# Kernel tuning notes

Hardware: AMD Instinct MI355X
Metric: run time of the kernel (lower is better)

The kernel has to match this reference:

```python
import jax, jax.numpy as jnp
import numpy as np

BATCH = 262144
LATENT_DIM = 128
N_CLUSTERS = 10


def setup_inputs() -> dict:
    key = jax.random.key(0)
    kz, kc = jax.random.split(key)
    z = jax.random.normal(kz, (BATCH, LATENT_DIM), dtype=jnp.float32)
    cluster_centers = jax.random.normal(kc, (N_CLUSTERS, LATENT_DIM), dtype=jnp.float32)
    return {"z": z, "cluster_centers": cluster_centers}


def reference(z, cluster_centers):
    # Student's-t soft assignment (alpha = 1):
    # q_ij = (1 + ||z_i - mu_j||^2)^-1, power ((alpha+1)/2) == 1
    # squared distances: [B, K]
    sq_dist = jnp.sum(jnp.square(z[:, None, :] - cluster_centers[None, :, :]), axis=2)
    q = 1.0 / (1.0 + sq_dist)
    q = q ** ((1.0 + 1.0) / 2.0)
    q = q / jnp.sum(q, axis=1, keepdims=True)  # row-normalize

    # target distribution p
    weight = q ** 2 / jnp.sum(q, axis=0)            # [B, K] / [K]
    p = weight / jnp.sum(weight, axis=1, keepdims=True)
    return (q, p)
```

## Files before the change

kernel.cpp:

```cpp
#include <hip/hip_runtime.h>
#include <stdint.h>

#define NB 262144
#define D 128
#define K 10

#define QBLOCKS 2048
#define QTHREADS 256
#define QITERS (NB * 4 / (QBLOCKS * QTHREADS))

__global__ __launch_bounds__(QTHREADS) void qkern(
    const float* __restrict__ z, const float* __restrict__ centers,
    float* __restrict__ qout, float* __restrict__ f) {
  __shared__ float c_lds[K * D];
  __shared__ float red[4][K];

  const int t = threadIdx.x;
  const int w = t >> 6;
  const int lane = t & 63;

  for (int i = t; i < K * D; i += QTHREADS) c_lds[i] = centers[i];
  __syncthreads();

  float colp[K];
#pragma unroll
  for (int j = 0; j < K; ++j) colp[j] = 0.f;

  for (int it = 0; it < QITERS; ++it) {
    const int g = (blockIdx.x + it * QBLOCKS) * QTHREADS + t;
    const int r = g >> 2;
    const int sub = g & 3;

    float acc[K];
#pragma unroll
    for (int j = 0; j < K; ++j) acc[j] = 0.f;

    const float* zr = z + (size_t)r * D + sub * 4;
#pragma unroll
    for (int k = 0; k < 8; ++k) {
      float4 zv = *reinterpret_cast<const float4*>(&zr[k * 16]);
#pragma unroll
      for (int j = 0; j < K; ++j) {
        float4 cv = *reinterpret_cast<const float4*>(&c_lds[j * D + k * 16 + sub * 4]);
        float dx = zv.x - cv.x; acc[j] = fmaf(dx, dx, acc[j]);
        float dy = zv.y - cv.y; acc[j] = fmaf(dy, dy, acc[j]);
        float dz = zv.z - cv.z; acc[j] = fmaf(dz, dz, acc[j]);
        float dw = zv.w - cv.w; acc[j] = fmaf(dw, dw, acc[j]);
      }
    }
#pragma unroll
    for (int j = 0; j < K; ++j) {
      acc[j] += __shfl_xor(acc[j], 1);
      acc[j] += __shfl_xor(acc[j], 2);
    }

    if (sub == 0) {
      float qu[K];
      float srow = 0.f;
#pragma unroll
      for (int j = 0; j < K; ++j) {
        qu[j] = 1.0f / (1.0f + acc[j]);
        srow += qu[j];
      }
      float inv = 1.0f / srow;
#pragma unroll
      for (int j = 0; j < K; ++j) {
        qu[j] *= inv;
        colp[j] += qu[j];
      }
      float* qo = qout + (size_t)r * K;
      *reinterpret_cast<float4*>(&qo[0]) = make_float4(qu[0], qu[1], qu[2], qu[3]);
      *reinterpret_cast<float4*>(&qo[4]) = make_float4(qu[4], qu[5], qu[6], qu[7]);
      *reinterpret_cast<float2*>(&qo[8]) = make_float2(qu[8], qu[9]);
    }
  }

#pragma unroll
  for (int j = 0; j < K; ++j) {
    colp[j] += __shfl_xor(colp[j], 4);
    colp[j] += __shfl_xor(colp[j], 8);
    colp[j] += __shfl_xor(colp[j], 16);
    colp[j] += __shfl_xor(colp[j], 32);
  }
  if (lane == 0) {
#pragma unroll
    for (int j = 0; j < K; ++j) red[w][j] = colp[j];
  }
  __syncthreads();
  if (t < K) {
    float s = red[0][t] + red[1][t] + red[2][t] + red[3][t];
    atomicAdd(&f[t], s);
  }
}

__global__ __launch_bounds__(256) void pkern(
    const float* __restrict__ q, const float* __restrict__ f,
    float* __restrict__ p) {
  int row = blockIdx.x * 256 + threadIdx.x;
  const float* qr = q + (size_t)row * K;
  float wv[K];
  float s = 0.f;
#pragma unroll
  for (int j = 0; j < K; j += 2) {
    float2 qq = *reinterpret_cast<const float2*>(&qr[j]);
    wv[j] = qq.x * qq.x / f[j];
    wv[j + 1] = qq.y * qq.y / f[j + 1];
    s += wv[j] + wv[j + 1];
  }
  float inv = 1.0f / s;
  float* pr = p + (size_t)row * K;
#pragma unroll
  for (int j = 0; j < K; j += 2) {
    *reinterpret_cast<float2*>(&pr[j]) = make_float2(wv[j] * inv, wv[j + 1] * inv);
  }
}

extern "C" void kernel_launch(void* const* d_in, const int* in_sizes, int n_in,
                              void* d_out, int out_size, void* d_ws, size_t ws_size,
                              hipStream_t stream) {
  const float* z = (const float*)d_in[0];
  const float* centers = (const float*)d_in[1];
  float* out = (float*)d_out;
  float* f = (float*)d_ws;

  hipMemsetAsync(d_ws, 0, K * sizeof(float), stream);
  qkern<<<QBLOCKS, QTHREADS, 0, stream>>>(z, centers, out, f);
  pkern<<<NB / 256, 256, 0, stream>>>(out, f, out + (size_t)NB * K);
}
```

Measured before the change: 252.4 us.

## Compute cluster distances with bf16 MFMA via norm expansion

```diff
diff --git a/kernel.cpp b/kernel.cpp
--- a/kernel.cpp
+++ b/kernel.cpp
@@ -5,92 +5,112 @@
 #define D 128
 #define K 10
 
-#define QBLOCKS 2048
+#define QBLOCKS 1024
 #define QTHREADS 256
-#define QITERS (NB * 4 / (QBLOCKS * QTHREADS))
+#define ROWS_PER_BLOCK (NB / QBLOCKS)
+#define TILES_PER_WAVE (ROWS_PER_BLOCK / 4 / 16)
+
+typedef __attribute__((ext_vector_type(8))) __bf16 bf16x8;
+typedef __attribute__((ext_vector_type(4))) float f32x4;
+
+__device__ inline __bf16 f2bf(float x) {
+  unsigned u = __builtin_bit_cast(unsigned, x);
+  u += 0x7fffu + ((u >> 16) & 1u);
+  unsigned short s = (unsigned short)(u >> 16);
+  return __builtin_bit_cast(__bf16, s);
+}
+
+__device__ inline bf16x8 make_frag(float4 lo, float4 hi) {
+  bf16x8 a;
+  a[0] = f2bf(lo.x); a[1] = f2bf(lo.y); a[2] = f2bf(lo.z); a[3] = f2bf(lo.w);
+  a[4] = f2bf(hi.x); a[5] = f2bf(hi.y); a[6] = f2bf(hi.z); a[7] = f2bf(hi.w);
+  return a;
+}
 
 __global__ __launch_bounds__(QTHREADS) void qkern(
     const float* __restrict__ z, const float* __restrict__ centers,
     float* __restrict__ qout, float* __restrict__ f) {
-  __shared__ float c_lds[K * D];
-  __shared__ float red[4][K];
+  __shared__ float red[4][16];
 
   const int t = threadIdx.x;
   const int w = t >> 6;
   const int lane = t & 63;
+  const int n = lane & 15;
+  const int g = lane >> 4;
 
-  for (int i = t; i < K * D; i += QTHREADS) c_lds[i] = centers[i];
-  __syncthreads();
-
-  float colp[K];
+  bf16x8 bfrag[4];
+  float mu2 = 0.f;
+  if (n < K) {
+    const float* cp = centers + n * D;
 #pragma unroll
-  for (int j = 0; j < K; ++j) colp[j] = 0.f;
-
-  for (int it = 0; it < QITERS; ++it) {
-    const int g = (blockIdx.x + it * QBLOCKS) * QTHREADS + t;
-    const int r = g >> 2;
-    const int sub = g & 3;
-
-    float acc[K];
-#pragma unroll
-    for (int j = 0; j < K; ++j) acc[j] = 0.f;
-
-    const float* zr = z + (size_t)r * D + sub * 4;
-#pragma unroll
-    for (int k = 0; k < 8; ++k) {
-      float4 zv = *reinterpret_cast<const float4*>(&zr[k * 16]);
-#pragma unroll
-      for (int j = 0; j < K; ++j) {
-        float4 cv = *reinterpret_cast<const float4*>(&c_lds[j * D + k * 16 + sub * 4]);
-        float dx = zv.x - cv.x; acc[j] = fmaf(dx, dx, acc[j]);
-        float dy = zv.y - cv.y; acc[j] = fmaf(dy, dy, acc[j]);
-        float dz = zv.z - cv.z; acc[j] = fmaf(dz, dz, acc[j]);
-        float dw = zv.w - cv.w; acc[j] = fmaf(dw, dw, acc[j]);
-      }
+    for (int c = 0; c < 4; ++c) {
+      float4 lo = *reinterpret_cast<const float4*>(cp + c * 32 + g * 8);
+      float4 hi = *reinterpret_cast<const float4*>(cp + c * 32 + g * 8 + 4);
+      bfrag[c] = make_frag(lo, hi);
     }
 #pragma unroll
-    for (int j = 0; j < K; ++j) {
-      acc[j] += __shfl_xor(acc[j], 1);
-      acc[j] += __shfl_xor(acc[j], 2);
+    for (int d4 = 0; d4 < 32; ++d4) {
+      float4 v = *reinterpret_cast<const float4*>(cp + d4 * 4);
+      mu2 = fmaf(v.x, v.x, mu2); mu2 = fmaf(v.y, v.y, mu2);
+      mu2 = fmaf(v.z, v.z, mu2); mu2 = fmaf(v.w, v.w, mu2);
+    }
+  } else {
+    unsigned short zb = 0;
+#pragma unroll
+    for (int c = 0; c < 4; ++c)
+#pragma unroll
+      for (int j = 0; j < 8; ++j) bfrag[c][j] = __builtin_bit_cast(__bf16, zb);
+  }
+
+  float colp = 0.f;
+  const int wbase = blockIdx.x * ROWS_PER_BLOCK + w * (TILES_PER_WAVE * 16);
+
+  for (int tile = 0; tile < TILES_PER_WAVE; ++tile) {
+    const int rbase = wbase + tile * 16;
+    const float* zr = z + (size_t)(rbase + n) * D + g * 8;
+
+    float4 zf[8];
+#pragma unroll
+    for (int c = 0; c < 4; ++c) {
+      zf[2 * c]     = *reinterpret_cast<const float4*>(zr + c * 32);
+      zf[2 * c + 1] = *reinterpret_cast<const float4*>(zr + c * 32 + 4);
     }
 
-    if (sub == 0) {
-      float qu[K];
-      float srow = 0.f;
+    float z2 = 0.f;
 #pragma unroll
-      for (int j = 0; j < K; ++j) {
-        qu[j] = 1.0f / (1.0f + acc[j]);
-        srow += qu[j];
-      }
-      float inv = 1.0f / srow;
+    for (int q8 = 0; q8 < 8; ++q8) {
+      z2 = fmaf(zf[q8].x, zf[q8].x, z2); z2 = fmaf(zf[q8].y, zf[q8].y, z2);
+      z2 = fmaf(zf[q8].z, zf[q8].z, z2); z2 = fmaf(zf[q8].w, zf[q8].w, z2);
+    }
+    z2 += __shfl_xor(z2, 16);
+    z2 += __shfl_xor(z2, 32);
+
+    f32x4 acc = {0.f, 0.f, 0.f, 0.f};
 #pragma unroll
-      for (int j = 0; j < K; ++j) {
-        qu[j] *= inv;
-        colp[j] += qu[j];
-      }
-      float* qo = qout + (size_t)r * K;
-      *reinterpret_cast<float4*>(&qo[0]) = make_float4(qu[0], qu[1], qu[2], qu[3]);
-      *reinterpret_cast<float4*>(&qo[4]) = make_float4(qu[4], qu[5], qu[6], qu[7]);
-      *reinterpret_cast<float2*>(&qo[8]) = make_float2(qu[8], qu[9]);
+    for (int c = 0; c < 4; ++c) {
+      bf16x8 a = make_frag(zf[2 * c], zf[2 * c + 1]);
+      acc = __builtin_amdgcn_mfma_f32_16x16x32_bf16(a, bfrag[c], acc, 0, 0, 0);
+    }
+
+#pragma unroll
+    for (int i = 0; i < 4; ++i) {
+      float z2i = __shfl(z2, g * 4 + i);
+      float d2 = z2i - 2.f * acc[i] + mu2;
+      float qu = (n < K) ? 1.0f / (1.0f + d2) : 0.f;
+      float rs = qu;
+      rs += __shfl_xor(rs, 1); rs += __shfl_xor(rs, 2);
+      rs += __shfl_xor(rs, 4); rs += __shfl_xor(rs, 8);
+      float qv = qu * (1.0f / rs);
+      if (n < K) qout[(size_t)(rbase + g * 4 + i) * K + n] = qv;
+      colp += qv;
     }
   }
 
-#pragma unroll
-  for (int j = 0; j < K; ++j) {
-    colp[j] += __shfl_xor(colp[j], 4);
-    colp[j] += __shfl_xor(colp[j], 8);
-    colp[j] += __shfl_xor(colp[j], 16);
-    colp[j] += __shfl_xor(colp[j], 32);
-  }
-  if (lane == 0) {
-#pragma unroll
-    for (int j = 0; j < K; ++j) red[w][j] = colp[j];
-  }
+  colp += __shfl_xor(colp, 16);
+  colp += __shfl_xor(colp, 32);
+  if (lane < 16) red[w][lane] = colp;
   __syncthreads();
-  if (t < K) {
-    float s = red[0][t] + red[1][t] + red[2][t] + red[3][t];
-    atomicAdd(&f[t], s);
-  }
+  if (t < K) atomicAdd(&f[t], red[0][t] + red[1][t] + red[2][t] + red[3][t]);
 }
 
 __global__ __launch_bounds__(256) void pkern(
```

Measured after the change: 210.1 us. 16.8% less time.
